# Performance work log

Hardware: AMD Instinct MI355X
Metric: run time of the kernel (lower is better)

The kernel has to match this reference:

```python
import jax, jax.numpy as jnp
import numpy as np

N_NODES = 100000
N_EDGES = 1600000
IN_DIM = 128
OUT_DIM = 64


def setup_inputs() -> dict:
    key = jax.random.key(0)
    k = jax.random.split(key, 6)
    h = jax.random.normal(k[0], (N_NODES, IN_DIM), dtype=jnp.float32)
    W_fc = jax.random.normal(k[1], (IN_DIM, OUT_DIM), dtype=jnp.float32) / np.float32(np.sqrt(IN_DIM))
    W_attn = jax.random.normal(k[2], (2 * OUT_DIM, 1), dtype=jnp.float32) / np.float32(np.sqrt(2 * OUT_DIM))
    W_edge = jax.random.normal(k[3], (2 * OUT_DIM, OUT_DIM), dtype=jnp.float32) / np.float32(np.sqrt(2 * OUT_DIM))
    src = jax.random.randint(k[4], (N_EDGES,), 0, N_NODES, dtype=jnp.int32)
    dst = jax.random.randint(k[5], (N_EDGES,), 0, N_NODES, dtype=jnp.int32)
    return {"h": h, "W_fc": W_fc, "W_attn": W_attn, "W_edge": W_edge, "src": src, "dst": dst}


def reference(h, W_fc, W_attn, W_edge, src, dst):
    # node projection: z = fc(h)
    z = h @ W_fc                                   # [N, out_dim]
    # gather per-edge src/dst features and concat (edge_type == 0 branch)
    z2 = jnp.concatenate([z[src], z[dst]], axis=1)  # [E, 2*out_dim]
    a = (z2 @ W_attn)[:, 0]                         # [E] attention logits
    e = z2 @ W_edge                                 # [E, out_dim] edge messages
    # segment softmax over incoming edges of each destination node
    a_max = jax.ops.segment_max(a, dst, num_segments=N_NODES)   # [N]
    w = jnp.exp(a - a_max[dst])                                  # [E]
    denom = jax.ops.segment_sum(w, dst, num_segments=N_NODES)    # [N]
    alpha = w / denom[dst]                                       # [E]
    # weighted scatter-add of neighbor features + sum of edge messages
    h1 = jax.ops.segment_sum(alpha[:, None] * z[src], dst, num_segments=N_NODES)
    h2 = jax.ops.segment_sum(e, dst, num_segments=N_NODES)
    return h1 + h2
```

## Files before the change

kernel.cpp:

```cpp
#include <hip/hip_runtime.h>

#define IN_DIM 128
#define OUT_DIM 64

#define NB 256
#define BSHIFT 9
#define NPB 512
#define EPT 16

typedef __attribute__((ext_vector_type(8))) short short8;
typedef __attribute__((ext_vector_type(4))) float f32x4;

__device__ __forceinline__ unsigned pack_bf16x2(float a, float b) {
    unsigned ua = __float_as_uint(a), ub = __float_as_uint(b);
    ua = (ua + 0x7fffu + ((ua >> 16) & 1u)) >> 16;
    ub = (ub + 0x7fffu + ((ub >> 16) & 1u)) >> 16;
    return ua | (ub << 16);
}

__global__ void precompute_weights(const float* __restrict__ W_fc,
                                   const float* __restrict__ W_edge,
                                   float* __restrict__ W1, float* __restrict__ W2) {
    int k = blockIdx.x;
    int j = threadIdx.x;
    __shared__ float row[64];
    row[j] = W_fc[k * 64 + j];
    __syncthreads();
    float s1 = 0.f, s2 = 0.f;
    #pragma unroll 8
    for (int m = 0; m < 64; ++m) {
        float w = row[m];
        s1 = fmaf(w, W_edge[m * 64 + j], s1);
        s2 = fmaf(w, W_edge[(64 + m) * 64 + j], s2);
    }
    W1[k * 64 + j] = s1;
    W2[k * 64 + j] = s2;
}

__global__ void pack_bfrags(const float* __restrict__ W_fc, const float* __restrict__ W1,
                            const float* __restrict__ W2, unsigned* __restrict__ bfrag) {
    int slot = blockIdx.x * 256 + threadIdx.x;
    if (slot >= 12 * 4 * 64) return;
    int lane = slot & 63;
    int ks = (slot >> 6) & 3;
    int t = slot >> 8;
    int grp = t >> 2;
    int col = (t & 3) * 16 + (lane & 15);
    int kbase = ks * 32 + (lane >> 4) * 8;
    const float* W = (grp == 0) ? W_fc : ((grp == 1) ? W1 : W2);
    unsigned o0 = pack_bf16x2(W[(kbase + 0) * 64 + col], W[(kbase + 1) * 64 + col]);
    unsigned o1 = pack_bf16x2(W[(kbase + 2) * 64 + col], W[(kbase + 3) * 64 + col]);
    unsigned o2 = pack_bf16x2(W[(kbase + 4) * 64 + col], W[(kbase + 5) * 64 + col]);
    unsigned o3 = pack_bf16x2(W[(kbase + 6) * 64 + col], W[(kbase + 7) * 64 + col]);
    ((uint4*)bfrag)[slot] = make_uint4(o0, o1, o2, o3);
}

__global__ __launch_bounds__(256) void node_gemm(
    const float* __restrict__ h, const unsigned* __restrict__ bfrag,
    const float* __restrict__ W_attn,
    unsigned* __restrict__ zes, float* __restrict__ ed,
    float* __restrict__ ws_, int N)
{
    __shared__ uint4 lds4[1024];
    char* lds = (char*)lds4;
    const int tid = threadIdx.x;
    const int lane = tid & 63;
    const int w = tid >> 6;
    const int n0 = blockIdx.x * 64;

    #pragma unroll
    for (int r = 0; r < 8; ++r) {
        int idx = r * 256 + tid;
        int row = idx >> 5;
        int c4 = idx & 31;
        float4 v = make_float4(0.f, 0.f, 0.f, 0.f);
        int n = n0 + row;
        if (n < N) v = *(const float4*)(h + (size_t)n * IN_DIM + c4 * 4);
        int byte = (row << 8) + (c4 << 3);
        byte ^= ((row & 7) << 4);
        *(uint2*)(lds + byte) = make_uint2(pack_bf16x2(v.x, v.y), pack_bf16x2(v.z, v.w));
    }
    __syncthreads();

    const int g = lane >> 4;
    const int c = lane & 15;

    union U { uint4 u; short8 s; };
    U a[4];
    {
        const int arow = (w << 4) + c;
        #pragma unroll
        for (int ks = 0; ks < 4; ++ks) {
            int byte = (arow << 8) + (ks << 6) + (g << 4);
            byte ^= ((arow & 7) << 4);
            a[ks].u = *(const uint4*)(lds + byte);
        }
    }

    f32x4 acc[12];
    #pragma unroll
    for (int t = 0; t < 12; ++t) acc[t] = (f32x4){0.f, 0.f, 0.f, 0.f};

    const uint4* bf4 = (const uint4*)bfrag;
    #pragma unroll
    for (int t = 0; t < 12; ++t) {
        #pragma unroll
        for (int ks = 0; ks < 4; ++ks) {
            U b; b.u = bf4[(t * 4 + ks) * 64 + lane];
            acc[t] = __builtin_amdgcn_mfma_f32_16x16x32_bf16(a[ks].s, b.s, acc[t], 0, 0, 0);
        }
    }

    const float wa0 = W_attn[c], wa1 = W_attn[16 + c], wa2 = W_attn[32 + c], wa3 = W_attn[48 + c];
    #pragma unroll
    for (int r = 0; r < 4; ++r) {
        const int n = n0 + (w << 4) + (g << 2) + r;
        float part = acc[0][r] * wa0 + acc[1][r] * wa1 + acc[2][r] * wa2 + acc[3][r] * wa3;
        part += __shfl_xor(part, 1);
        part += __shfl_xor(part, 2);
        part += __shfl_xor(part, 4);
        part += __shfl_xor(part, 8);
        if (n <= N) {
            #pragma unroll
            for (int t = 0; t < 4; ++t) {
                const int col = t * 16 + c;
                zes[(size_t)n * 64 + col] = pack_bf16x2(acc[t][r], acc[t + 4][r]);
                ed [(size_t)n * 64 + col] = acc[t + 8][r];
            }
            if (c == 0) ws_[n] = expf(part);
        }
    }
}

__global__ __launch_bounds__(256) void coarse_hist(const int* __restrict__ dst,
                                                   unsigned* __restrict__ hist, int E) {
    __shared__ unsigned hl[NB];
    const int t = threadIdx.x;
    hl[t] = 0;
    __syncthreads();
    const int base = blockIdx.x * (256 * EPT);
    const int lim = min(base + 256 * EPT, E);
    for (int i = base + t; i < lim; i += 256)
        atomicAdd(&hl[((unsigned)dst[i]) >> BSHIFT], 1u);
    __syncthreads();
    if (hl[t]) atomicAdd(&hist[t], hl[t]);
}

__global__ void bucket_scan(const unsigned* __restrict__ hist,
                            unsigned* __restrict__ bucketBase, unsigned* __restrict__ cursor) {
    __shared__ unsigned s[NB];
    const int t = threadIdx.x;
    unsigned v = hist[t];
    s[t] = v; __syncthreads();
    for (int off = 1; off < NB; off <<= 1) {
        unsigned add = (t >= off) ? s[t - off] : 0u;
        __syncthreads();
        s[t] += add;
        __syncthreads();
    }
    unsigned excl = s[t] - v;
    bucketBase[t] = excl;
    cursor[t] = excl;
    if (t == NB - 1) bucketBase[NB] = s[t];
}

__global__ __launch_bounds__(256) void coarse_scatter(
    const int* __restrict__ src, const int* __restrict__ dst,
    unsigned* __restrict__ cursor, unsigned* __restrict__ pairs, int E)
{
    __shared__ unsigned h[NB];
    __shared__ unsigned start[NB];
    const int t = threadIdx.x;
    h[t] = 0;
    __syncthreads();
    const int base = blockIdx.x * (256 * EPT);
    unsigned pv[EPT], bk[EPT], rk[EPT];
    #pragma unroll
    for (int k = 0; k < EPT; ++k) {
        int i = base + k * 256 + t;
        bool valid = i < E;
        unsigned s = 0, d = 0;
        if (valid) { s = (unsigned)src[i]; d = (unsigned)dst[i]; }
        pv[k] = (s << BSHIFT) | (d & (NPB - 1));
        bk[k] = valid ? (d >> BSHIFT) : 0xFFFFFFFFu;
        rk[k] = valid ? atomicAdd(&h[d >> BSHIFT], 1u) : 0u;
    }
    __syncthreads();
    start[t] = h[t] ? atomicAdd(&cursor[t], h[t]) : 0u;
    __syncthreads();
    #pragma unroll
    for (int k = 0; k < EPT; ++k) {
        if (bk[k] != 0xFFFFFFFFu)
            pairs[start[bk[k]] + rk[k]] = pv[k];
    }
}

__global__ __launch_bounds__(256) void fine_bin(
    const unsigned* __restrict__ pairs, const unsigned* __restrict__ bucketBase,
    unsigned* __restrict__ offs, int* __restrict__ srcoff_sorted, int N, int E)
{
    __shared__ unsigned deg[NPB];
    __shared__ unsigned excl[NPB];
    __shared__ unsigned pscan[256];
    const int b = blockIdx.x;
    const int t = threadIdx.x;
    const int node0 = b << BSHIFT;
    const unsigned e0 = bucketBase[b], e1 = bucketBase[b + 1];

    deg[t] = 0; deg[t + 256] = 0;
    __syncthreads();
    for (unsigned i = e0 + t; i < e1; i += 256)
        atomicAdd(&deg[pairs[i] & (NPB - 1)], 1u);
    __syncthreads();

    unsigned a0 = deg[2 * t], a1 = deg[2 * t + 1];
    unsigned ps = a0 + a1;
    pscan[t] = ps;
    __syncthreads();
    for (int off = 1; off < 256; off <<= 1) {
        unsigned add = (t >= off) ? pscan[t - off] : 0u;
        __syncthreads();
        pscan[t] += add;
        __syncthreads();
    }
    unsigned exclP = pscan[t] - ps;
    excl[2 * t] = exclP;
    excl[2 * t + 1] = exclP + a0;
    __syncthreads();

    #pragma unroll
    for (int l = t; l < NPB; l += 256) {
        int n = node0 + l;
        if (n < N) offs[n] = e0 + excl[l];
    }
    if (b == 0 && t == 0) offs[N] = (unsigned)E;
    __syncthreads();

    for (unsigned i = e0 + t; i < e1; i += 256) {
        unsigned p = pairs[i];
        unsigned loc = p & (NPB - 1);
        unsigned pos = e0 + atomicAdd(&excl[loc], 1u);
        srcoff_sorted[pos] = (int)((p >> BSHIFT) << 8);
    }
}

__global__ __launch_bounds__(256) void gather_nodes(
    const int* __restrict__ srcoff_sorted, const unsigned* __restrict__ offs,
    const float* __restrict__ ws_, const unsigned* __restrict__ zes,
    const float* __restrict__ ed, float* __restrict__ out, int N)
{
    const int lane = threadIdx.x & 63;
    const int goff4 = (lane >> 4) << 2;
    const int c4off = (lane & 15) << 4;
    const int d = blockIdx.x * 4 + (threadIdx.x >> 6);
    if (d >= N) return;
    const unsigned o0 = offs[d], o1 = offs[d + 1];
    const int deg = (int)(o1 - o0);
    const int zoff = N << 8;
    const char* zesb = (const char*)zes;

    float az0 = 0.f, az1 = 0.f, az2 = 0.f, az3 = 0.f;
    float ae0 = 0.f, ae1 = 0.f, ae2 = 0.f, ae3 = 0.f;
    float lsum = 0.f;

    for (unsigned o = o0; o < o1; o += 64) {
        const int rem = min(64, (int)(o1 - o));
        int soff = zoff; float w = 0.f;
        if (lane < rem) { soff = srcoff_sorted[o + lane]; w = ws_[(unsigned)soff >> 8]; }
        lsum += w;
        for (int j = 0; j < rem; j += 16) {
            int so[4]; float wg[4];
            #pragma unroll
            for (int k = 0; k < 4; ++k) {
                const int idx4 = ((j + 4 * k) << 2) + goff4;
                so[k] = __builtin_amdgcn_ds_bpermute(idx4, soff);
                wg[k] = __uint_as_float(
                    (unsigned)__builtin_amdgcn_ds_bpermute(idx4, (int)__float_as_uint(w)));
            }
            uint4 u[4];
            #pragma unroll
            for (int k = 0; k < 4; ++k)
                u[k] = *(const uint4*)(zesb + (unsigned)(so[k] + c4off));
            #pragma unroll
            for (int k = 0; k < 4; ++k) {
                az0 = fmaf(wg[k], __uint_as_float(u[k].x << 16), az0); ae0 += __uint_as_float(u[k].x & 0xffff0000u);
                az1 = fmaf(wg[k], __uint_as_float(u[k].y << 16), az1); ae1 += __uint_as_float(u[k].y & 0xffff0000u);
                az2 = fmaf(wg[k], __uint_as_float(u[k].z << 16), az2); ae2 += __uint_as_float(u[k].z & 0xffff0000u);
                az3 = fmaf(wg[k], __uint_as_float(u[k].w << 16), az3); ae3 += __uint_as_float(u[k].w & 0xffff0000u);
            }
        }
    }

    az0 += __shfl_xor(az0, 16); az0 += __shfl_xor(az0, 32);
    az1 += __shfl_xor(az1, 16); az1 += __shfl_xor(az1, 32);
    az2 += __shfl_xor(az2, 16); az2 += __shfl_xor(az2, 32);
    az3 += __shfl_xor(az3, 16); az3 += __shfl_xor(az3, 32);
    ae0 += __shfl_xor(ae0, 16); ae0 += __shfl_xor(ae0, 32);
    ae1 += __shfl_xor(ae1, 16); ae1 += __shfl_xor(ae1, 32);
    ae2 += __shfl_xor(ae2, 16); ae2 += __shfl_xor(ae2, 32);
    ae3 += __shfl_xor(ae3, 16); ae3 += __shfl_xor(ae3, 32);
    #pragma unroll
    for (int off = 32; off; off >>= 1) lsum += __shfl_xor(lsum, off);

    if (goff4 == 0) {
        const float inv = (lsum > 0.f) ? 1.f / lsum : 0.f;
        const float4 edv = *(const float4*)&ed[(size_t)d * 64 + (c4off >> 2)];
        float4 r;
        r.x = fmaf((float)deg, edv.x, fmaf(az0, inv, ae0));
        r.y = fmaf((float)deg, edv.y, fmaf(az1, inv, ae1));
        r.z = fmaf((float)deg, edv.z, fmaf(az2, inv, ae2));
        r.w = fmaf((float)deg, edv.w, fmaf(az3, inv, ae3));
        *(float4*)&out[(size_t)d * 64 + (c4off >> 2)] = r;
    }
}

extern "C" void kernel_launch(void* const* d_in, const int* in_sizes, int n_in,
                              void* d_out, int out_size, void* d_ws, size_t ws_size,
                              hipStream_t stream) {
    const float* h      = (const float*)d_in[0];
    const float* W_fc   = (const float*)d_in[1];
    const float* W_attn = (const float*)d_in[2];
    const float* W_edge = (const float*)d_in[3];
    const int*   src    = (const int*)d_in[4];
    const int*   dst    = (const int*)d_in[5];
    float* out = (float*)d_out;

    const int N = in_sizes[0] / IN_DIM;
    const int E = in_sizes[4];

    char* p = (char*)d_ws;
    auto alloc = [&](size_t bytes) -> void* {
        void* r = (void*)p;
        p += (bytes + 255) & ~(size_t)255;
        return r;
    };
    unsigned* zes    = (unsigned*)alloc((size_t)(N + 1) * 64 * 4);
    float*    ed     = (float*)alloc((size_t)(N + 1) * 64 * 4);
    float*    ws_    = (float*)alloc((size_t)(N + 1) * 4);
    unsigned* offs   = (unsigned*)alloc((size_t)(N + 1) * 4);
    unsigned* hist   = (unsigned*)alloc(NB * 4);
    unsigned* bbase  = (unsigned*)alloc((NB + 1) * 4);
    unsigned* cursor = (unsigned*)alloc(NB * 4);
    unsigned* pairs  = (unsigned*)alloc((size_t)E * 4);
    int*      src_s  = (int*)alloc((size_t)E * 4);
    float*    W1     = (float*)alloc(128 * 64 * 4);
    float*    W2     = (float*)alloc(128 * 64 * 4);
    unsigned* bfrag  = (unsigned*)alloc((size_t)12 * 4 * 64 * 16);

    hipMemsetAsync(hist, 0, NB * 4, stream);

    precompute_weights<<<128, 64, 0, stream>>>(W_fc, W_edge, W1, W2);
    pack_bfrags<<<12, 256, 0, stream>>>(W_fc, W1, W2, bfrag);

    int blocksA = (N + 63) / 64;
    node_gemm<<<blocksA, 256, 0, stream>>>(h, bfrag, W_attn, zes, ed, ws_, N);

    int blocksC = (E + 256 * EPT - 1) / (256 * EPT);
    coarse_hist<<<blocksC, 256, 0, stream>>>(dst, hist, E);
    bucket_scan<<<1, NB, 0, stream>>>(hist, bbase, cursor);
    coarse_scatter<<<blocksC, 256, 0, stream>>>(src, dst, cursor, pairs, E);
    fine_bin<<<NB, 256, 0, stream>>>(pairs, bbase, offs, src_s, N, E);

    gather_nodes<<<(N + 3) / 4, 256, 0, stream>>>(src_s, offs, ws_, zes, ed, out, N);
}
```

Baseline: 251.4 us.

## Assign one 16-lane group per destination node in gather kernel

The gather kernel now maps each destination node to a 16-lane quarter-wave instead of a full 64-lane wave, so each block handles 16 nodes. With an average degree of about 16, the old mapping left most lanes idle in the edge loop and needed a cross-group reduction at the end. Now each group loads up to 16 edges at a time and steps through them 4 at a time, with no final feature reduction. The trade-off is that the lanes of a wave work on nodes with different degrees, so they diverge, and each lane carries a longer serial chain of accumulations.

Measured after the change: 252.5 us. About the same (+0.5%).

```diff
diff --git a/kernel.cpp b/kernel.cpp
--- a/kernel.cpp
+++ b/kernel.cpp
@@ -250,9 +250,10 @@
     const float* __restrict__ ed, float* __restrict__ out, int N)
 {
     const int lane = threadIdx.x & 63;
-    const int goff4 = (lane >> 4) << 2;
-    const int c4off = (lane & 15) << 4;
-    const int d = blockIdx.x * 4 + (threadIdx.x >> 6);
+    const int l16 = lane & 15;
+    const int gbase4 = (lane & 48) << 2;
+    const int c4off = l16 << 4;
+    const int d = blockIdx.x * 16 + (threadIdx.x >> 4);
     if (d >= N) return;
     const unsigned o0 = offs[d], o1 = offs[d + 1];
     const int deg = (int)(o1 - o0);
@@ -263,16 +264,17 @@
     float ae0 = 0.f, ae1 = 0.f, ae2 = 0.f, ae3 = 0.f;
     float lsum = 0.f;
 
-    for (unsigned o = o0; o < o1; o += 64) {
-        const int rem = min(64, (int)(o1 - o));
+    for (unsigned base = o0; base < o1; base += 16) {
+        const int rem = min(16, (int)(o1 - base));
         int soff = zoff; float w = 0.f;
-        if (lane < rem) { soff = srcoff_sorted[o + lane]; w = ws_[(unsigned)soff >> 8]; }
+        if (l16 < rem) { soff = srcoff_sorted[base + l16]; w = ws_[(unsigned)soff >> 8]; }
         lsum += w;
-        for (int j = 0; j < rem; j += 16) {
+        const int e_end = (rem + 3) & ~3;
+        for (int e = 0; e < e_end; e += 4) {
             int so[4]; float wg[4];
             #pragma unroll
             for (int k = 0; k < 4; ++k) {
-                const int idx4 = ((j + 4 * k) << 2) + goff4;
+                const int idx4 = gbase4 + ((e + k) << 2);
                 so[k] = __builtin_amdgcn_ds_bpermute(idx4, soff);
                 wg[k] = __uint_as_float(
                     (unsigned)__builtin_amdgcn_ds_bpermute(idx4, (int)__float_as_uint(w)));
@@ -291,27 +293,19 @@
         }
     }
 
-    az0 += __shfl_xor(az0, 16); az0 += __shfl_xor(az0, 32);
-    az1 += __shfl_xor(az1, 16); az1 += __shfl_xor(az1, 32);
-    az2 += __shfl_xor(az2, 16); az2 += __shfl_xor(az2, 32);
-    az3 += __shfl_xor(az3, 16); az3 += __shfl_xor(az3, 32);
-    ae0 += __shfl_xor(ae0, 16); ae0 += __shfl_xor(ae0, 32);
-    ae1 += __shfl_xor(ae1, 16); ae1 += __shfl_xor(ae1, 32);
-    ae2 += __shfl_xor(ae2, 16); ae2 += __shfl_xor(ae2, 32);
-    ae3 += __shfl_xor(ae3, 16); ae3 += __shfl_xor(ae3, 32);
-    #pragma unroll
-    for (int off = 32; off; off >>= 1) lsum += __shfl_xor(lsum, off);
-
-    if (goff4 == 0) {
-        const float inv = (lsum > 0.f) ? 1.f / lsum : 0.f;
-        const float4 edv = *(const float4*)&ed[(size_t)d * 64 + (c4off >> 2)];
-        float4 r;
-        r.x = fmaf((float)deg, edv.x, fmaf(az0, inv, ae0));
-        r.y = fmaf((float)deg, edv.y, fmaf(az1, inv, ae1));
-        r.z = fmaf((float)deg, edv.z, fmaf(az2, inv, ae2));
-        r.w = fmaf((float)deg, edv.w, fmaf(az3, inv, ae3));
-        *(float4*)&out[(size_t)d * 64 + (c4off >> 2)] = r;
-    }
+    lsum += __shfl_xor(lsum, 1);
+    lsum += __shfl_xor(lsum, 2);
+    lsum += __shfl_xor(lsum, 4);
+    lsum += __shfl_xor(lsum, 8);
+
+    const float inv = (lsum > 0.f) ? 1.f / lsum : 0.f;
+    const float4 edv = *(const float4*)&ed[(size_t)d * 64 + l16 * 4];
+    float4 r;
+    r.x = fmaf((float)deg, edv.x, fmaf(az0, inv, ae0));
+    r.y = fmaf((float)deg, edv.y, fmaf(az1, inv, ae1));
+    r.z = fmaf((float)deg, edv.z, fmaf(az2, inv, ae2));
+    r.w = fmaf((float)deg, edv.w, fmaf(az3, inv, ae3));
+    *(float4*)&out[(size_t)d * 64 + l16 * 4] = r;
 }
 
 extern "C" void kernel_launch(void* const* d_in, const int* in_sizes, int n_in,
@@ -361,5 +355,5 @@
     coarse_scatter<<<blocksC, 256, 0, stream>>>(src, dst, cursor, pairs, E);
     fine_bin<<<NB, 256, 0, stream>>>(pairs, bbase, offs, src_s, N, E);
 
-    gather_nodes<<<(N + 3) / 4, 256, 0, stream>>>(src_s, offs, ws_, zes, ed, out, N);
-}
+    gather_nodes<<<(N + 15) / 16, 256, 0, stream>>>(src_s, offs, ws_, zes, ed, out, N);
+}
```
